# Kernel tuning notes

Measured on AMD Instinct MI355X. Metric: run time of the kernel, lower is better.

The kernel has to match this reference:

```python
import jax, jax.numpy as jnp
import numpy as np

B = 512       # number of graphs in the batch
MAXL = 128    # max nodes per graph (pad length)
H = 512       # hidden_features


def setup_inputs() -> dict:
    rng = np.random.default_rng(0)
    lengths = rng.integers(1, MAXL + 1, size=B)  # num nodes per graph, >=1
    N = int(lengths.sum())
    key = jax.random.key(0)
    ks = jax.random.split(key, 12)
    s = 1.0 / np.sqrt(H)
    u = lambda k, shape: jax.random.uniform(k, shape, jnp.float32, -s, s)
    return dict(
        h=jax.random.normal(ks[0], (N, H), jnp.float32),
        lengths=jnp.asarray(lengths, jnp.int32),
        bias=u(ks[1], (H,)),
        w_ih_f=u(ks[2], (3 * H, H)), w_hh_f=u(ks[3], (3 * H, H)),
        b_ih_f=u(ks[4], (3 * H,)), b_hh_f=u(ks[5], (3 * H,)),
        w_ih_b=u(ks[6], (3 * H, H)), w_hh_b=u(ks[7], (3 * H, H)),
        b_ih_b=u(ks[8], (3 * H,)), b_hh_b=u(ks[9], (3 * H,)),
    )


def _gru_scan(x_tbh, h0, w_ih, w_hh, b_ih, b_hh, reverse):
    # Precompute all input-gate projections in one GEMM: [T,B,3H]
    gx = jnp.einsum('tbh,gh->tbg', x_tbh, w_ih) + b_ih

    def step(hc, g):
        gh = hc @ w_hh.T + b_hh
        r = jax.nn.sigmoid(g[:, :H] + gh[:, :H])
        z = jax.nn.sigmoid(g[:, H:2 * H] + gh[:, H:2 * H])
        n = jnp.tanh(g[:, 2 * H:] + r * gh[:, 2 * H:])
        hn = (1.0 - z) * n + z * hc
        return hn, hn

    _, out = jax.lax.scan(step, h0, gx, reverse=reverse)
    return out  # [T,B,H], aligned with input time order


def reference(h, lengths, bias, w_ih_f, w_hh_f, b_ih_f, b_hh_f,
              w_ih_b, w_hh_b, b_ih_b, b_hh_b):
    lengths_np = np.asarray(lengths)
    starts = np.concatenate([[0], np.cumsum(lengths_np)[:-1]])
    seg = np.repeat(np.arange(B), lengths_np)            # [N] graph id per node
    pos = np.arange(seg.shape[0]) - starts[seg]          # [N] position within graph

    message = jax.nn.relu(h + bias)                      # [N,H]
    h0 = jax.ops.segment_max(h, seg, num_segments=B)     # per-graph max-pool init [B,H]

    # Pad ragged node features into [B, MAXL, H] (zeros beyond length, like ZeroPad2d)
    padded = jnp.zeros((B, MAXL, H), h.dtype).at[seg, pos].set(message)
    x = padded.transpose(1, 0, 2)                        # [T,B,H]

    # Bidirectional GRU; both directions start from the max-pool hidden.
    # Note: torch runs the plain (non-packed) GRU over the zero padding too,
    # so the reverse direction consumes padding before real tokens — replicated here.
    out_f = _gru_scan(x, h0, w_ih_f, w_hh_f, b_ih_f, b_hh_f, reverse=False)
    out_b = _gru_scan(x, h0, w_ih_b, w_hh_b, b_ih_b, b_hh_b, reverse=True)
    out = jnp.concatenate([out_f, out_b], axis=-1).transpose(1, 0, 2)  # [B,T,2H]

    node_out = out[seg, pos]                             # unpad -> [N,2H]
    sums = jax.ops.segment_sum(node_out, seg, num_segments=B)
    return sums / jnp.asarray(lengths_np, sums.dtype)[:, None]  # mean_nodes [B,2H]
```

## Files before the change

### kernel.cpp

```cpp
#include <hip/hip_runtime.h>
#include <hip/hip_bf16.h>
#include <math.h>

#define BATCH 512
#define MAXL 128
#define HID 512
#define H3 1536

typedef __bf16 bf16x8 __attribute__((ext_vector_type(8)));
typedef __bf16 bf16x4 __attribute__((ext_vector_type(4)));
typedef float f32x4 __attribute__((ext_vector_type(4)));

__global__ __launch_bounds__(BATCH) void scan_kernel(const int* __restrict__ len,
                                                     int* __restrict__ starts,
                                                     unsigned* __restrict__ ctr) {
    __shared__ int buf[BATCH];
    int tid = threadIdx.x;
    ctr[tid] = 0u;
    int myLen = len[tid];
    buf[tid] = myLen;
    __syncthreads();
    for (int off = 1; off < BATCH; off <<= 1) {
        int v = (tid >= off) ? buf[tid - off] : 0;
        __syncthreads();
        buf[tid] += v;
        __syncthreads();
    }
    starts[tid] = buf[tid] - myLen;
}

__global__ __launch_bounds__(HID) void init_kernel(const float* __restrict__ h,
                                                   const int* __restrict__ len,
                                                   const int* __restrict__ starts,
                                                   float* __restrict__ h0,
                                                   __bf16* __restrict__ hb) {
    int b = blockIdx.x, j = threadIdx.x;
    int s = starts[b], L = len[b];
    float m = -3.4e38f;
    for (int t = 0; t < L; ++t) m = fmaxf(m, h[(size_t)(s + t) * HID + j]);
    h0[(size_t)b * HID + j] = m;
    hb[(size_t)b * HID + j] = (__bf16)m;
    hb[(size_t)(BATCH + b) * HID + j] = (__bf16)m;
}

__global__ void msg_kernel(const float* __restrict__ h, const float* __restrict__ bias,
                           __bf16* __restrict__ msg, long total4) {
    for (long i = (long)blockIdx.x * blockDim.x + threadIdx.x; i < total4;
         i += (long)gridDim.x * blockDim.x) {
        float4 v = ((const float4*)h)[i];
        int c4 = (int)(i & (HID / 4 - 1));
        float4 bb = ((const float4*)bias)[c4];
        bf16x4 o;
        o[0] = (__bf16)fmaxf(v.x + bb.x, 0.f);
        o[1] = (__bf16)fmaxf(v.y + bb.y, 0.f);
        o[2] = (__bf16)fmaxf(v.z + bb.z, 0.f);
        o[3] = (__bf16)fmaxf(v.w + bb.w, 0.f);
        ((bf16x4*)msg)[i] = o;
    }
}

__global__ void conv_kernel(const float* __restrict__ src, __bf16* __restrict__ dst, int n4) {
    int i = blockIdx.x * blockDim.x + threadIdx.x;
    if (i < n4) {
        float4 v = ((const float4*)src)[i];
        bf16x4 o;
        o[0] = (__bf16)v.x; o[1] = (__bf16)v.y; o[2] = (__bf16)v.z; o[3] = (__bf16)v.w;
        ((bf16x4*)dst)[i] = o;
    }
}

__global__ __launch_bounds__(256) void gx_gemm(const __bf16* __restrict__ msg,
                                               const __bf16* __restrict__ wih,
                                               __bf16* __restrict__ gx,
                                               int N) {
    __shared__ __bf16 alds[64 * 512];
    __shared__ __bf16 tile[64][136];
    int dir = blockIdx.y;
    int r0 = blockIdx.x * 64;
    int wid = threadIdx.x >> 6, lane = threadIdx.x & 63;
    int lrow = lane & 15, lk = lane >> 4;
    const __bf16* wB = wih + (size_t)dir * H3 * HID;
    __bf16* gOut = gx + (size_t)dir * N * H3;

    for (int i = threadIdx.x; i < 64 * 64; i += 256) {
        int row = i >> 6, ch = i & 63;
        int sch = ch ^ (row & 7);
        int grow = r0 + row; if (grow >= N) grow = N - 1;
        *(bf16x8*)(&alds[row * 512 + sch * 8]) = *(const bf16x8*)(msg + (size_t)grow * HID + ch * 8);
    }
    __syncthreads();

    for (int ct = 0; ct < 12; ++ct) {
        int c0 = ct * 128 + wid * 32;
        f32x4 acc[4][2] = {};
#pragma unroll
        for (int ks = 0; ks < 16; ++ks) {
            bf16x8 b0 = *(const bf16x8*)(wB + (size_t)(c0 + lrow) * HID + ks * 32 + lk * 8);
            bf16x8 b1 = *(const bf16x8*)(wB + (size_t)(c0 + 16 + lrow) * HID + ks * 32 + lk * 8);
#pragma unroll
            for (int rf = 0; rf < 4; ++rf) {
                int row = rf * 16 + lrow;
                int sch = (ks * 4 + lk) ^ (row & 7);
                bf16x8 av = *(const bf16x8*)(&alds[row * 512 + sch * 8]);
                acc[rf][0] = __builtin_amdgcn_mfma_f32_16x16x32_bf16(av, b0, acc[rf][0], 0, 0, 0);
                acc[rf][1] = __builtin_amdgcn_mfma_f32_16x16x32_bf16(av, b1, acc[rf][1], 0, 0, 0);
            }
        }
        __syncthreads();
#pragma unroll
        for (int rf = 0; rf < 4; ++rf)
#pragma unroll
            for (int fj = 0; fj < 2; ++fj)
#pragma unroll
                for (int r = 0; r < 4; ++r)
                    tile[rf * 16 + (lane >> 4) * 4 + r][wid * 32 + fj * 16 + (lane & 15)] =
                        (__bf16)acc[rf][fj][r];
        __syncthreads();
        int row = threadIdx.x >> 2, ch = threadIdx.x & 3;
        if (r0 + row < N) {
            __bf16* d = gOut + (size_t)(r0 + row) * H3 + ct * 128 + ch * 32;
            *(bf16x8*)(d)      = *(const bf16x8*)(&tile[row][ch * 32]);
            *(bf16x8*)(d + 8)  = *(const bf16x8*)(&tile[row][ch * 32 + 8]);
            *(bf16x8*)(d + 16) = *(const bf16x8*)(&tile[row][ch * 32 + 16]);
            *(bf16x8*)(d + 24) = *(const bf16x8*)(&tile[row][ch * 32 + 24]);
        }
    }
}

__global__ __launch_bounds__(256, 1) void gru_scan(
    const __bf16* __restrict__ whh,
    const __bf16* __restrict__ gx,
    const float* __restrict__ h0,
    __bf16* __restrict__ hb,
    const float* __restrict__ b_ih_f, const float* __restrict__ b_hh_f,
    const float* __restrict__ b_ih_b, const float* __restrict__ b_hh_b,
    const int* __restrict__ len, const int* __restrict__ starts,
    unsigned* __restrict__ ctr,
    float* __restrict__ out, int N) {

    __shared__ __bf16 wlds[96 * 512];
    __shared__ __bf16 hout[64 * 40];

    int bid = blockIdx.x;
    int rg  = bid & 7;
    int dir = (bid >> 3) & 1;
    int hc  = bid >> 4;
    int grp = dir * 8 + rg;
    int wid = threadIdx.x >> 6, lane = threadIdx.x & 63;
    int r0 = rg * 64;
    int c0 = hc * 32;

    for (int i = threadIdx.x; i < 96 * 64; i += 256) {
        int row = i >> 6, ch = i & 63;
        int g = row >> 5, c = row & 31;
        int sch = ch ^ (row & 7);
        const __bf16* src = whh + ((size_t)dir * H3 + (size_t)g * HID + c0 + c) * HID + ch * 8;
        *(bf16x8*)(&wlds[row * 512 + sch * 8]) = *(const bf16x8*)src;
    }

    int wr0 = r0 + wid * 16;
    int lrow = lane & 15;
    int lk   = lane >> 4;

    int mycol[2], myrow[4];
#pragma unroll
    for (int fj = 0; fj < 2; ++fj) mycol[fj] = c0 + fj * 16 + (lane & 15);
#pragma unroll
    for (int r = 0; r < 4; ++r) myrow[r] = wr0 + (lane >> 4) * 4 + r;

    float hreg[2][4], sreg[2][4];
#pragma unroll
    for (int fj = 0; fj < 2; ++fj)
#pragma unroll
        for (int r = 0; r < 4; ++r) {
            hreg[fj][r] = h0[(size_t)myrow[r] * HID + mycol[fj]];
            sreg[fj][r] = 0.f;
        }

    const float* bih = dir ? b_ih_b : b_ih_f;
    const float* bhh = dir ? b_hh_b : b_hh_f;
    float bihv[2][3], bhhv[2][3];
#pragma unroll
    for (int fj = 0; fj < 2; ++fj)
#pragma unroll
        for (int g = 0; g < 3; ++g) {
            bihv[fj][g] = bih[g * HID + mycol[fj]];
            bhhv[fj][g] = bhh[g * HID + mycol[fj]];
        }
    int mylen[4], mystart[4];
#pragma unroll
    for (int r = 0; r < 4; ++r) { mylen[r] = len[myrow[r]]; mystart[r] = starts[myrow[r]]; }

    float gxv[2][4][3];
    {
        int t = dir ? (MAXL - 1) : 0;
#pragma unroll
        for (int r = 0; r < 4; ++r) {
            bool real = t < mylen[r];
            size_t base = ((size_t)dir * N + mystart[r] + t) * H3;
#pragma unroll
            for (int fj = 0; fj < 2; ++fj)
#pragma unroll
                for (int g = 0; g < 3; ++g)
                    gxv[fj][r][g] = real ? (float)gx[base + (size_t)g * HID + mycol[fj]] : 0.f;
        }
    }

    __syncthreads();

    const size_t bufStride = (size_t)2 * BATCH * HID;

    for (int s = 0; s < MAXL; ++s) {
        int t = dir ? (MAXL - 1 - s) : s;
        const __bf16* hcur = hb + (size_t)(s & 1) * bufStride + (size_t)dir * BATCH * HID;
        __bf16* hnxt = hb + (size_t)((s + 1) & 1) * bufStride + (size_t)dir * BATCH * HID;

        bf16x8 a[16];
#pragma unroll
        for (int ks = 0; ks < 16; ++ks) {
            const __bf16* p = hcur + (size_t)(wr0 + lrow) * HID + ks * 32 + lk * 8;
            asm volatile("global_load_dwordx4 %0, %1, off sc0 sc1"
                         : "=v"(a[ks]) : "v"((const void*)p) : "memory");
        }
        asm volatile("s_waitcnt vmcnt(0)" ::: "memory");
        __builtin_amdgcn_sched_barrier(0);

        f32x4 acc[3][2] = {};
#pragma unroll
        for (int ks = 0; ks < 16; ++ks) {
#pragma unroll
            for (int g = 0; g < 3; ++g) {
#pragma unroll
                for (int f = 0; f < 2; ++f) {
                    int row = g * 32 + f * 16 + lrow;
                    int sch = (ks * 4 + lk) ^ (row & 7);
                    bf16x8 b = *(const bf16x8*)(&wlds[row * 512 + sch * 8]);
                    acc[g][f] = __builtin_amdgcn_mfma_f32_16x16x32_bf16(a[ks], b, acc[g][f], 0, 0, 0);
                }
            }
        }

#pragma unroll
        for (int fj = 0; fj < 2; ++fj)
#pragma unroll
            for (int r = 0; r < 4; ++r) {
                float ghr = acc[0][fj][r] + bhhv[fj][0];
                float ghz = acc[1][fj][r] + bhhv[fj][1];
                float ghn = acc[2][fj][r] + bhhv[fj][2];
                float xr = gxv[fj][r][0] + bihv[fj][0];
                float xz = gxv[fj][r][1] + bihv[fj][1];
                float xn = gxv[fj][r][2] + bihv[fj][2];
                float rg_ = 1.f / (1.f + expf(-(xr + ghr)));
                float zg  = 1.f / (1.f + expf(-(xz + ghz)));
                float ng  = tanhf(xn + rg_ * ghn);
                float hn  = (1.f - zg) * ng + zg * hreg[fj][r];
                hreg[fj][r] = hn;
                if (t < mylen[r]) sreg[fj][r] += hn;
            }

#pragma unroll
        for (int fj = 0; fj < 2; ++fj)
#pragma unroll
            for (int r = 0; r < 4; ++r)
                hout[(wid * 16 + (lane >> 4) * 4 + r) * 40 + fj * 16 + (lane & 15)] =
                    (__bf16)hreg[fj][r];
        __syncthreads();
        {
            int row = threadIdx.x >> 2, ch = threadIdx.x & 3;
            __bf16* dst = hnxt + (size_t)(r0 + row) * HID + c0 + ch * 8;
            bf16x8 v = *(const bf16x8*)(&hout[row * 40 + ch * 8]);
            asm volatile("global_store_dwordx4 %0, %1, off sc0 sc1"
                         :: "v"((void*)dst), "v"(v) : "memory");
        }
        if (s + 1 == MAXL) break;

        asm volatile("s_waitcnt vmcnt(0)" ::: "memory");
        __syncthreads();
        if (threadIdx.x == 0)
            __hip_atomic_store(ctr + grp * 16 + hc, (unsigned)(s + 1),
                               __ATOMIC_RELAXED, __HIP_MEMORY_SCOPE_AGENT);

        {
            int tn = dir ? (MAXL - 2 - s) : (s + 1);
#pragma unroll
            for (int r = 0; r < 4; ++r) {
                bool real = tn < mylen[r];
                size_t base = ((size_t)dir * N + mystart[r] + tn) * H3;
#pragma unroll
                for (int fj = 0; fj < 2; ++fj)
#pragma unroll
                    for (int g = 0; g < 3; ++g)
                        gxv[fj][r][g] = real ? (float)gx[base + (size_t)g * HID + mycol[fj]] : 0.f;
            }
        }

        if (threadIdx.x < 16) {
            unsigned tgt = (unsigned)(s + 1);
            while (__hip_atomic_load(ctr + grp * 16 + threadIdx.x, __ATOMIC_RELAXED,
                                     __HIP_MEMORY_SCOPE_AGENT) < tgt)
                __builtin_amdgcn_s_sleep(1);
        }
        __syncthreads();
        asm volatile("" ::: "memory");
        __builtin_amdgcn_sched_barrier(0);
    }

#pragma unroll
    for (int fj = 0; fj < 2; ++fj)
#pragma unroll
        for (int r = 0; r < 4; ++r)
            out[(size_t)myrow[r] * (2 * HID) + (size_t)dir * HID + mycol[fj]] =
                sreg[fj][r] / (float)mylen[r];
}

extern "C" void kernel_launch(void* const* d_in, const int* in_sizes, int n_in,
                              void* d_out, int out_size, void* d_ws, size_t ws_size,
                              hipStream_t stream) {
    const float* h      = (const float*)d_in[0];
    const int*   lens   = (const int*)d_in[1];
    const float* bias   = (const float*)d_in[2];
    const float* w_ih_f = (const float*)d_in[3];
    const float* w_hh_f = (const float*)d_in[4];
    const float* b_ih_f = (const float*)d_in[5];
    const float* b_hh_f = (const float*)d_in[6];
    const float* w_ih_b = (const float*)d_in[7];
    const float* w_hh_b = (const float*)d_in[8];
    const float* b_ih_b = (const float*)d_in[9];
    const float* b_hh_b = (const float*)d_in[10];
    float* out = (float*)d_out;
    const int N = in_sizes[0] / HID;

    char* p = (char*)d_ws;
    size_t off = 0;
    int* starts   = (int*)(p + off);        off += 4096;
    unsigned* ctr = (unsigned*)(p + off);   off += 4096;
    float* h0   = (float*)(p + off);        off += (size_t)BATCH * HID * 4;
    __bf16* hb  = (__bf16*)(p + off);       off += (size_t)2 * 2 * BATCH * HID * 2;
    __bf16* wih = (__bf16*)(p + off);       off += (size_t)2 * H3 * HID * 2;
    __bf16* whh = (__bf16*)(p + off);       off += (size_t)2 * H3 * HID * 2;
    __bf16* msg = (__bf16*)(p + off);       off += (size_t)N * HID * 2;
    __bf16* gx  = (__bf16*)(p + off);       off += (size_t)2 * N * H3 * 2;
    if (off > ws_size) return;

    scan_kernel<<<1, BATCH, 0, stream>>>(lens, starts, ctr);
    init_kernel<<<BATCH, HID, 0, stream>>>(h, lens, starts, h0, hb);

    long total4 = (long)N * HID / 4;
    int msgBlocks = (int)((total4 + 255) / 256); if (msgBlocks > 2048) msgBlocks = 2048;
    msg_kernel<<<msgBlocks, 256, 0, stream>>>(h, bias, msg, total4);

    int n4 = H3 * HID / 4;
    int cb = (n4 + 255) / 256;
    conv_kernel<<<cb, 256, 0, stream>>>(w_ih_f, wih, n4);
    conv_kernel<<<cb, 256, 0, stream>>>(w_ih_b, wih + (size_t)H3 * HID, n4);
    conv_kernel<<<cb, 256, 0, stream>>>(w_hh_f, whh, n4);
    conv_kernel<<<cb, 256, 0, stream>>>(w_hh_b, whh + (size_t)H3 * HID, n4);

    gx_gemm<<<dim3((N + 63) / 64, 2), 256, 0, stream>>>(msg, wih, gx, N);

    int Nv = N;
    void* kargs[] = {(void*)&whh, (void*)&gx, (void*)&h0, (void*)&hb,
                     (void*)&b_ih_f, (void*)&b_hh_f, (void*)&b_ih_b, (void*)&b_hh_b,
                     (void*)&lens, (void*)&starts, (void*)&ctr, (void*)&out, (void*)&Nv};
    hipLaunchCooperativeKernel((const void*)gru_scan, dim3(256), dim3(256), kargs, 0, stream);
}
```

Before: 1.832 ms.

## Interleave two independent row groups per block to overlap cross-block sync latency

Each block now owns 16 hidden columns for two separate batch row groups instead of 32 columns for one. It alternates between them: it computes and publishes group 0's step, then waits on group 1's flags and computes it. The aim is to hide the global spin-wait and flag-propagation latency of one group behind the other group's MFMA and gate work. It also halves the weight tile held in LDS. In exchange each step adds an extra barrier and flag round, and the counter layout changes to 32 flags per group, which must match the unseen launch and setup code.

```diff
diff --git a/kernel.cpp b/kernel.cpp
--- a/kernel.cpp
+++ b/kernel.cpp
@@ -10,6 +10,28 @@
 typedef __bf16 bf16x8 __attribute__((ext_vector_type(8)));
 typedef __bf16 bf16x4 __attribute__((ext_vector_type(4)));
 typedef float f32x4 __attribute__((ext_vector_type(4)));
+
+__device__ __forceinline__ bf16x8 ld_coh16(const __bf16* p) {
+    bf16x8 v;
+    asm volatile("global_load_dwordx4 %0, %1, off sc0 sc1"
+                 : "=v"(v) : "v"((const void*)p) : "memory");
+    return v;
+}
+__device__ __forceinline__ void st_coh16(__bf16* p, bf16x8 v) {
+    asm volatile("global_store_dwordx4 %0, %1, off sc0 sc1"
+                 :: "v"((void*)p), "v"(v) : "memory");
+}
+__device__ __forceinline__ void st_coh4(unsigned* p, unsigned v) {
+    asm volatile("global_store_dword %0, %1, off sc0 sc1"
+                 :: "v"((void*)p), "v"(v) : "memory");
+}
+__device__ __forceinline__ unsigned ld_coh4(const unsigned* p) {
+    unsigned v;
+    asm volatile("global_load_dword %0, %1, off sc0 sc1"
+                 : "=v"(v) : "v"((const void*)p) : "memory");
+    asm volatile("s_waitcnt vmcnt(0)" ::: "memory");
+    return v;
+}
 
 __global__ __launch_bounds__(BATCH) void scan_kernel(const int* __restrict__ len,
                                                      int* __restrict__ starts,
@@ -138,71 +160,75 @@
     unsigned* __restrict__ ctr,
     float* __restrict__ out, int N) {
 
-    __shared__ __bf16 wlds[96 * 512];
-    __shared__ __bf16 hout[64 * 40];
+    __shared__ __bf16 wlds[48 * 512];
+    __shared__ __bf16 hout[64 * 24];
 
     int bid = blockIdx.x;
-    int rg  = bid & 7;
-    int dir = (bid >> 3) & 1;
-    int hc  = bid >> 4;
-    int grp = dir * 8 + rg;
+    int rgp = bid & 3;
+    int dir = (bid >> 2) & 1;
+    int hc  = bid >> 3;
+    int c0  = hc * 16;
+    int g0  = dir * 8 + rgp;
+    int g1  = g0 + 4;
+    int r0_0 = rgp * 64;
+    int r0_1 = (rgp + 4) * 64;
     int wid = threadIdx.x >> 6, lane = threadIdx.x & 63;
-    int r0 = rg * 64;
-    int c0 = hc * 32;
-
-    for (int i = threadIdx.x; i < 96 * 64; i += 256) {
+    int lrow = lane & 15, lk = lane >> 4;
+
+    for (int i = threadIdx.x; i < 48 * 64; i += 256) {
         int row = i >> 6, ch = i & 63;
-        int g = row >> 5, c = row & 31;
+        int g = row >> 4, c = row & 15;
         int sch = ch ^ (row & 7);
         const __bf16* src = whh + ((size_t)dir * H3 + (size_t)g * HID + c0 + c) * HID + ch * 8;
         *(bf16x8*)(&wlds[row * 512 + sch * 8]) = *(const bf16x8*)src;
     }
 
-    int wr0 = r0 + wid * 16;
-    int lrow = lane & 15;
-    int lk   = lane >> 4;
-
-    int mycol[2], myrow[4];
-#pragma unroll
-    for (int fj = 0; fj < 2; ++fj) mycol[fj] = c0 + fj * 16 + (lane & 15);
-#pragma unroll
-    for (int r = 0; r < 4; ++r) myrow[r] = wr0 + (lane >> 4) * 4 + r;
-
-    float hreg[2][4], sreg[2][4];
-#pragma unroll
-    for (int fj = 0; fj < 2; ++fj)
-#pragma unroll
-        for (int r = 0; r < 4; ++r) {
-            hreg[fj][r] = h0[(size_t)myrow[r] * HID + mycol[fj]];
-            sreg[fj][r] = 0.f;
-        }
+    int wr0_0 = r0_0 + wid * 16;
+    int wr0_1 = r0_1 + wid * 16;
+    int mycol = c0 + lrow;
+    int myrow0[4], myrow1[4];
+#pragma unroll
+    for (int r = 0; r < 4; ++r) {
+        myrow0[r] = wr0_0 + lk * 4 + r;
+        myrow1[r] = wr0_1 + lk * 4 + r;
+    }
+
+    float hreg0[4], hreg1[4], sreg0[4], sreg1[4];
+#pragma unroll
+    for (int r = 0; r < 4; ++r) {
+        hreg0[r] = h0[(size_t)myrow0[r] * HID + mycol];
+        hreg1[r] = h0[(size_t)myrow1[r] * HID + mycol];
+        sreg0[r] = 0.f; sreg1[r] = 0.f;
+    }
 
     const float* bih = dir ? b_ih_b : b_ih_f;
     const float* bhh = dir ? b_hh_b : b_hh_f;
-    float bihv[2][3], bhhv[2][3];
-#pragma unroll
-    for (int fj = 0; fj < 2; ++fj)
-#pragma unroll
-        for (int g = 0; g < 3; ++g) {
-            bihv[fj][g] = bih[g * HID + mycol[fj]];
-            bhhv[fj][g] = bhh[g * HID + mycol[fj]];
-        }
-    int mylen[4], mystart[4];
-#pragma unroll
-    for (int r = 0; r < 4; ++r) { mylen[r] = len[myrow[r]]; mystart[r] = starts[myrow[r]]; }
-
-    float gxv[2][4][3];
+    float bihv[3], bhhv[3];
+#pragma unroll
+    for (int g = 0; g < 3; ++g) {
+        bihv[g] = bih[g * HID + mycol];
+        bhhv[g] = bhh[g * HID + mycol];
+    }
+    int mylen0[4], mystart0[4], mylen1[4], mystart1[4];
+#pragma unroll
+    for (int r = 0; r < 4; ++r) {
+        mylen0[r] = len[myrow0[r]]; mystart0[r] = starts[myrow0[r]];
+        mylen1[r] = len[myrow1[r]]; mystart1[r] = starts[myrow1[r]];
+    }
+
+    float gxv0[4][3], gxv1[4][3];
     {
         int t = dir ? (MAXL - 1) : 0;
 #pragma unroll
         for (int r = 0; r < 4; ++r) {
-            bool real = t < mylen[r];
-            size_t base = ((size_t)dir * N + mystart[r] + t) * H3;
-#pragma unroll
-            for (int fj = 0; fj < 2; ++fj)
-#pragma unroll
-                for (int g = 0; g < 3; ++g)
-                    gxv[fj][r][g] = real ? (float)gx[base + (size_t)g * HID + mycol[fj]] : 0.f;
+            bool re0 = t < mylen0[r], re1 = t < mylen1[r];
+            size_t b0 = ((size_t)dir * N + mystart0[r] + t) * H3;
+            size_t b1 = ((size_t)dir * N + mystart1[r] + t) * H3;
+#pragma unroll
+            for (int g = 0; g < 3; ++g) {
+                gxv0[r][g] = re0 ? (float)gx[b0 + (size_t)g * HID + mycol] : 0.f;
+                gxv1[r][g] = re1 ? (float)gx[b1 + (size_t)g * HID + mycol] : 0.f;
+            }
         }
     }
 
@@ -214,103 +240,142 @@
         int t = dir ? (MAXL - 1 - s) : s;
         const __bf16* hcur = hb + (size_t)(s & 1) * bufStride + (size_t)dir * BATCH * HID;
         __bf16* hnxt = hb + (size_t)((s + 1) & 1) * bufStride + (size_t)dir * BATCH * HID;
+        bool notLast = (s + 1 < MAXL);
+
+        if (s) {
+            if (threadIdx.x < 32) {
+                unsigned tgt = (unsigned)s;
+                while (ld_coh4(ctr + g0 * 32 + threadIdx.x) < tgt)
+                    __builtin_amdgcn_s_sleep(1);
+            }
+            __syncthreads();
+            asm volatile("" ::: "memory");
+            __builtin_amdgcn_sched_barrier(0);
+        }
 
         bf16x8 a[16];
 #pragma unroll
-        for (int ks = 0; ks < 16; ++ks) {
-            const __bf16* p = hcur + (size_t)(wr0 + lrow) * HID + ks * 32 + lk * 8;
-            asm volatile("global_load_dwordx4 %0, %1, off sc0 sc1"
-                         : "=v"(a[ks]) : "v"((const void*)p) : "memory");
-        }
+        for (int ks = 0; ks < 16; ++ks)
+            a[ks] = ld_coh16(hcur + (size_t)(wr0_0 + lrow) * HID + ks * 32 + lk * 8);
         asm volatile("s_waitcnt vmcnt(0)" ::: "memory");
         __builtin_amdgcn_sched_barrier(0);
 
-        f32x4 acc[3][2] = {};
+        f32x4 acc[3] = {};
 #pragma unroll
         for (int ks = 0; ks < 16; ++ks) {
 #pragma unroll
             for (int g = 0; g < 3; ++g) {
-#pragma unroll
-                for (int f = 0; f < 2; ++f) {
-                    int row = g * 32 + f * 16 + lrow;
-                    int sch = (ks * 4 + lk) ^ (row & 7);
-                    bf16x8 b = *(const bf16x8*)(&wlds[row * 512 + sch * 8]);
-                    acc[g][f] = __builtin_amdgcn_mfma_f32_16x16x32_bf16(a[ks], b, acc[g][f], 0, 0, 0);
+                int row = g * 16 + lrow;
+                int sch = (ks * 4 + lk) ^ (row & 7);
+                bf16x8 b = *(const bf16x8*)(&wlds[row * 512 + sch * 8]);
+                acc[g] = __builtin_amdgcn_mfma_f32_16x16x32_bf16(a[ks], b, acc[g], 0, 0, 0);
+            }
+        }
+#pragma unroll
+        for (int r = 0; r < 4; ++r) {
+            float ghr = acc[0][r] + bhhv[0];
+            float ghz = acc[1][r] + bhhv[1];
+            float ghn = acc[2][r] + bhhv[2];
+            float rg_ = 1.f / (1.f + expf(-(gxv0[r][0] + bihv[0] + ghr)));
+            float zg  = 1.f / (1.f + expf(-(gxv0[r][1] + bihv[1] + ghz)));
+            float ng  = tanhf(gxv0[r][2] + bihv[2] + rg_ * ghn);
+            float hn  = (1.f - zg) * ng + zg * hreg0[r];
+            hreg0[r] = hn;
+            if (t < mylen0[r]) sreg0[r] += hn;
+        }
+        if (notLast) {
+#pragma unroll
+            for (int r = 0; r < 4; ++r)
+                hout[(wid * 16 + lk * 4 + r) * 24 + lrow] = (__bf16)hreg0[r];
+            __syncthreads();
+            if (threadIdx.x < 128) {
+                int row = threadIdx.x >> 1, half = threadIdx.x & 1;
+                st_coh16(hnxt + (size_t)(r0_0 + row) * HID + c0 + half * 8,
+                         *(const bf16x8*)(&hout[row * 24 + half * 8]));
+            }
+            asm volatile("s_waitcnt vmcnt(0)" ::: "memory");
+            __syncthreads();
+            if (threadIdx.x == 0) st_coh4(ctr + g0 * 32 + hc, (unsigned)(s + 1));
+        }
+
+        if (s) {
+            if (threadIdx.x < 32) {
+                unsigned tgt = (unsigned)s;
+                while (ld_coh4(ctr + g1 * 32 + threadIdx.x) < tgt)
+                    __builtin_amdgcn_s_sleep(1);
+            }
+            __syncthreads();
+            asm volatile("" ::: "memory");
+            __builtin_amdgcn_sched_barrier(0);
+        } else {
+            __syncthreads();
+        }
+
+#pragma unroll
+        for (int ks = 0; ks < 16; ++ks)
+            a[ks] = ld_coh16(hcur + (size_t)(wr0_1 + lrow) * HID + ks * 32 + lk * 8);
+        asm volatile("s_waitcnt vmcnt(0)" ::: "memory");
+        __builtin_amdgcn_sched_barrier(0);
+
+        f32x4 acc1[3] = {};
+#pragma unroll
+        for (int ks = 0; ks < 16; ++ks) {
+#pragma unroll
+            for (int g = 0; g < 3; ++g) {
+                int row = g * 16 + lrow;
+                int sch = (ks * 4 + lk) ^ (row & 7);
+                bf16x8 b = *(const bf16x8*)(&wlds[row * 512 + sch * 8]);
+                acc1[g] = __builtin_amdgcn_mfma_f32_16x16x32_bf16(a[ks], b, acc1[g], 0, 0, 0);
+            }
+        }
+#pragma unroll
+        for (int r = 0; r < 4; ++r) {
+            float ghr = acc1[0][r] + bhhv[0];
+            float ghz = acc1[1][r] + bhhv[1];
+            float ghn = acc1[2][r] + bhhv[2];
+            float rg_ = 1.f / (1.f + expf(-(gxv1[r][0] + bihv[0] + ghr)));
+            float zg  = 1.f / (1.f + expf(-(gxv1[r][1] + bihv[1] + ghz)));
+            float ng  = tanhf(gxv1[r][2] + bihv[2] + rg_ * ghn);
+            float hn  = (1.f - zg) * ng + zg * hreg1[r];
+            hreg1[r] = hn;
+            if (t < mylen1[r]) sreg1[r] += hn;
+        }
+        if (notLast) {
+#pragma unroll
+            for (int r = 0; r < 4; ++r)
+                hout[(wid * 16 + lk * 4 + r) * 24 + lrow] = (__bf16)hreg1[r];
+            __syncthreads();
+            if (threadIdx.x < 128) {
+                int row = threadIdx.x >> 1, half = threadIdx.x & 1;
+                st_coh16(hnxt + (size_t)(r0_1 + row) * HID + c0 + half * 8,
+                         *(const bf16x8*)(&hout[row * 24 + half * 8]));
+            }
+            asm volatile("s_waitcnt vmcnt(0)" ::: "memory");
+            __syncthreads();
+            if (threadIdx.x == 0) st_coh4(ctr + g1 * 32 + hc, (unsigned)(s + 1));
+
+            int tn = dir ? (MAXL - 2 - s) : (s + 1);
+#pragma unroll
+            for (int r = 0; r < 4; ++r) {
+                bool re0 = tn < mylen0[r], re1 = tn < mylen1[r];
+                size_t b0 = ((size_t)dir * N + mystart0[r] + tn) * H3;
+                size_t b1 = ((size_t)dir * N + mystart1[r] + tn) * H3;
+#pragma unroll
+                for (int g = 0; g < 3; ++g) {
+                    gxv0[r][g] = re0 ? (float)gx[b0 + (size_t)g * HID + mycol] : 0.f;
+                    gxv1[r][g] = re1 ? (float)gx[b1 + (size_t)g * HID + mycol] : 0.f;
                 }
             }
         }
-
-#pragma unroll
-        for (int fj = 0; fj < 2; ++fj)
-#pragma unroll
-            for (int r = 0; r < 4; ++r) {
-                float ghr = acc[0][fj][r] + bhhv[fj][0];
-                float ghz = acc[1][fj][r] + bhhv[fj][1];
-                float ghn = acc[2][fj][r] + bhhv[fj][2];
-                float xr = gxv[fj][r][0] + bihv[fj][0];
-                float xz = gxv[fj][r][1] + bihv[fj][1];
-                float xn = gxv[fj][r][2] + bihv[fj][2];
-                float rg_ = 1.f / (1.f + expf(-(xr + ghr)));
-                float zg  = 1.f / (1.f + expf(-(xz + ghz)));
-                float ng  = tanhf(xn + rg_ * ghn);
-                float hn  = (1.f - zg) * ng + zg * hreg[fj][r];
-                hreg[fj][r] = hn;
-                if (t < mylen[r]) sreg[fj][r] += hn;
-            }
-
-#pragma unroll
-        for (int fj = 0; fj < 2; ++fj)
-#pragma unroll
-            for (int r = 0; r < 4; ++r)
-                hout[(wid * 16 + (lane >> 4) * 4 + r) * 40 + fj * 16 + (lane & 15)] =
-                    (__bf16)hreg[fj][r];
-        __syncthreads();
-        {
-            int row = threadIdx.x >> 2, ch = threadIdx.x & 3;
-            __bf16* dst = hnxt + (size_t)(r0 + row) * HID + c0 + ch * 8;
-            bf16x8 v = *(const bf16x8*)(&hout[row * 40 + ch * 8]);
-            asm volatile("global_store_dwordx4 %0, %1, off sc0 sc1"
-                         :: "v"((void*)dst), "v"(v) : "memory");
-        }
-        if (s + 1 == MAXL) break;
-
-        asm volatile("s_waitcnt vmcnt(0)" ::: "memory");
-        __syncthreads();
-        if (threadIdx.x == 0)
-            __hip_atomic_store(ctr + grp * 16 + hc, (unsigned)(s + 1),
-                               __ATOMIC_RELAXED, __HIP_MEMORY_SCOPE_AGENT);
-
-        {
-            int tn = dir ? (MAXL - 2 - s) : (s + 1);
-#pragma unroll
-            for (int r = 0; r < 4; ++r) {
-                bool real = tn < mylen[r];
-                size_t base = ((size_t)dir * N + mystart[r] + tn) * H3;
-#pragma unroll
-                for (int fj = 0; fj < 2; ++fj)
-#pragma unroll
-                    for (int g = 0; g < 3; ++g)
-                        gxv[fj][r][g] = real ? (float)gx[base + (size_t)g * HID + mycol[fj]] : 0.f;
-            }
-        }
-
-        if (threadIdx.x < 16) {
-            unsigned tgt = (unsigned)(s + 1);
-            while (__hip_atomic_load(ctr + grp * 16 + threadIdx.x, __ATOMIC_RELAXED,
-                                     __HIP_MEMORY_SCOPE_AGENT) < tgt)
-                __builtin_amdgcn_s_sleep(1);
-        }
-        __syncthreads();
-        asm volatile("" ::: "memory");
-        __builtin_amdgcn_sched_barrier(0);
-    }
-
-#pragma unroll
-    for (int fj = 0; fj < 2; ++fj)
-#pragma unroll
-        for (int r = 0; r < 4; ++r)
-            out[(size_t)myrow[r] * (2 * HID) + (size_t)dir * HID + mycol[fj]] =
-                sreg[fj][r] / (float)mylen[r];
+    }
+
+#pragma unroll
+    for (int r = 0; r < 4; ++r) {
+        out[(size_t)myrow0[r] * (2 * HID) + (size_t)dir * HID + mycol] =
+            sreg0[r] / (float)mylen0[r];
+        out[(size_t)myrow1[r] * (2 * HID) + (size_t)dir * HID + mycol] =
+            sreg1[r] / (float)mylen1[r];
+    }
 }
 
 extern "C" void kernel_launch(void* const* d_in, const int* in_sizes, int n_in,
```

New measurement: 2.488 ms. 35.8% more time.

## Replace block-wide barriers with per-wave flags in GRU recurrence

Applied to the files above, without the earlier changes.

Each wave now stages its own 16-row slice of the new hidden state in a private LDS buffer, stores it to global memory itself, and publishes a per-wave arrival counter. Each wave then polls only the 16 counters for its row slice across all column blocks, using a ballot. This removes the two __syncthreads per step and the block-level gather so waves advance independently. In exchange there are four times as many flag stores and polls, more traffic on the counter array, and the final step's store is skipped.

```diff
diff --git a/kernel.cpp b/kernel.cpp
--- a/kernel.cpp
+++ b/kernel.cpp
@@ -10,6 +10,28 @@
 typedef __bf16 bf16x8 __attribute__((ext_vector_type(8)));
 typedef __bf16 bf16x4 __attribute__((ext_vector_type(4)));
 typedef float f32x4 __attribute__((ext_vector_type(4)));
+
+__device__ __forceinline__ bf16x8 ld_coh16(const __bf16* p) {
+    bf16x8 v;
+    asm volatile("global_load_dwordx4 %0, %1, off sc0 sc1"
+                 : "=v"(v) : "v"((const void*)p) : "memory");
+    return v;
+}
+__device__ __forceinline__ void st_coh16(__bf16* p, bf16x8 v) {
+    asm volatile("global_store_dwordx4 %0, %1, off sc0 sc1"
+                 :: "v"((void*)p), "v"(v) : "memory");
+}
+__device__ __forceinline__ void st_coh4(unsigned* p, unsigned v) {
+    asm volatile("global_store_dword %0, %1, off sc0 sc1"
+                 :: "v"((void*)p), "v"(v) : "memory");
+}
+__device__ __forceinline__ unsigned ld_coh4(const unsigned* p) {
+    unsigned v;
+    asm volatile("global_load_dword %0, %1, off sc0 sc1"
+                 : "=v"(v) : "v"((const void*)p) : "memory");
+    asm volatile("s_waitcnt vmcnt(0)" ::: "memory");
+    return v;
+}
 
 __global__ __launch_bounds__(BATCH) void scan_kernel(const int* __restrict__ len,
                                                      int* __restrict__ starts,
@@ -17,6 +39,7 @@
     __shared__ int buf[BATCH];
     int tid = threadIdx.x;
     ctr[tid] = 0u;
+    ctr[tid + BATCH] = 0u;
     int myLen = len[tid];
     buf[tid] = myLen;
     __syncthreads();
@@ -139,7 +162,7 @@
     float* __restrict__ out, int N) {
 
     __shared__ __bf16 wlds[96 * 512];
-    __shared__ __bf16 hout[64 * 40];
+    __shared__ __bf16 hout[4][16 * 40];
 
     int bid = blockIdx.x;
     int rg  = bid & 7;
@@ -209,6 +232,9 @@
     __syncthreads();
 
     const size_t bufStride = (size_t)2 * BATCH * HID;
+    const size_t stoff = (size_t)(wr0 + (lane >> 2)) * HID + c0 + (lane & 3) * 8;
+    unsigned* myArrive = ctr + grp * 64 + wid * 16 + hc;
+    const unsigned* myPoll = ctr + grp * 64 + wid * 16 + (lane & 15);
 
     for (int s = 0; s < MAXL; ++s) {
         int t = dir ? (MAXL - 1 - s) : s;
@@ -217,11 +243,8 @@
 
         bf16x8 a[16];
 #pragma unroll
-        for (int ks = 0; ks < 16; ++ks) {
-            const __bf16* p = hcur + (size_t)(wr0 + lrow) * HID + ks * 32 + lk * 8;
-            asm volatile("global_load_dwordx4 %0, %1, off sc0 sc1"
-                         : "=v"(a[ks]) : "v"((const void*)p) : "memory");
-        }
+        for (int ks = 0; ks < 16; ++ks)
+            a[ks] = ld_coh16(hcur + (size_t)(wr0 + lrow) * HID + ks * 32 + lk * 8);
         asm volatile("s_waitcnt vmcnt(0)" ::: "memory");
         __builtin_amdgcn_sched_barrier(0);
 
@@ -258,27 +281,19 @@
                 if (t < mylen[r]) sreg[fj][r] += hn;
             }
 
+        if (s + 1 == MAXL) break;
+
 #pragma unroll
         for (int fj = 0; fj < 2; ++fj)
 #pragma unroll
             for (int r = 0; r < 4; ++r)
-                hout[(wid * 16 + (lane >> 4) * 4 + r) * 40 + fj * 16 + (lane & 15)] =
-                    (__bf16)hreg[fj][r];
-        __syncthreads();
+                hout[wid][(lk * 4 + r) * 40 + fj * 16 + lrow] = (__bf16)hreg[fj][r];
         {
-            int row = threadIdx.x >> 2, ch = threadIdx.x & 3;
-            __bf16* dst = hnxt + (size_t)(r0 + row) * HID + c0 + ch * 8;
-            bf16x8 v = *(const bf16x8*)(&hout[row * 40 + ch * 8]);
-            asm volatile("global_store_dwordx4 %0, %1, off sc0 sc1"
-                         :: "v"((void*)dst), "v"(v) : "memory");
-        }
-        if (s + 1 == MAXL) break;
-
+            bf16x8 v = *(const bf16x8*)(&hout[wid][(lane >> 2) * 40 + (lane & 3) * 8]);
+            st_coh16(hnxt + stoff, v);
+        }
         asm volatile("s_waitcnt vmcnt(0)" ::: "memory");
-        __syncthreads();
-        if (threadIdx.x == 0)
-            __hip_atomic_store(ctr + grp * 16 + hc, (unsigned)(s + 1),
-                               __ATOMIC_RELAXED, __HIP_MEMORY_SCOPE_AGENT);
+        if (lane == 0) st_coh4(myArrive, (unsigned)(s + 1));
 
         {
             int tn = dir ? (MAXL - 2 - s) : (s + 1);
@@ -294,13 +309,14 @@
             }
         }
 
-        if (threadIdx.x < 16) {
+        {
             unsigned tgt = (unsigned)(s + 1);
-            while (__hip_atomic_load(ctr + grp * 16 + threadIdx.x, __ATOMIC_RELAXED,
-                                     __HIP_MEMORY_SCOPE_AGENT) < tgt)
+            for (;;) {
+                unsigned v = ld_coh4(myPoll);
+                if (__ballot(v < tgt) == 0ull) break;
                 __builtin_amdgcn_s_sleep(1);
-        }
-        __syncthreads();
+            }
+        }
         asm volatile("" ::: "memory");
         __builtin_amdgcn_sched_barrier(0);
     }
```

After: 1.877 ms. 1.02x slower.
